# Kernel optimization log

Hardware: AMD Instinct MI355X
Metric: run time of the kernel (lower is better)

The kernel has to match this reference:

```python
import jax, jax.numpy as jnp
import numpy as np

D_MODEL = 1024
N_HEADS = 16
HEAD_DIM = D_MODEL // N_HEADS


def setup_inputs() -> dict:
    key = jax.random.key(0)
    ks = jax.random.split(key, 6)
    B, S = 2, 2048
    scale = 1.0 / np.sqrt(D_MODEL)
    x = jax.random.normal(ks[0], (B, S, D_MODEL), dtype=jnp.float32)
    Wq = jax.random.normal(ks[1], (D_MODEL, D_MODEL), dtype=jnp.float32) * scale
    Wk = jax.random.normal(ks[2], (D_MODEL, D_MODEL), dtype=jnp.float32) * scale
    Wv = jax.random.normal(ks[3], (D_MODEL, D_MODEL), dtype=jnp.float32) * scale
    Wo = jax.random.normal(ks[4], (D_MODEL, D_MODEL), dtype=jnp.float32) * scale
    bo = jax.random.normal(ks[5], (D_MODEL,), dtype=jnp.float32) * 0.02
    return {"x": x, "Wq": Wq, "Wk": Wk, "Wv": Wv, "Wo": Wo, "bo": bo}


def reference(x, Wq, Wk, Wv, Wo, bo):
    B, S, _ = x.shape
    H, hd = N_HEADS, HEAD_DIM
    # qkv projections (no bias, qkv_bias=False)
    q = (x @ Wq).reshape(B, S, H, hd).transpose(0, 2, 1, 3)  # [B,H,S,hd]
    k = (x @ Wk).reshape(B, S, H, hd).transpose(0, 2, 1, 3)
    v = (x @ Wv).reshape(B, S, H, hd).transpose(0, 2, 1, 3)
    scores = jnp.einsum('bhqd,bhkd->bhqk', q, k)  # [B,H,S,S]
    causal = jnp.tril(jnp.ones((S, S), dtype=bool))  # True = keep
    scores = jnp.where(causal, scores, -jnp.inf)
    weights = jax.nn.softmax(scores / np.sqrt(hd), axis=-1)
    # dropout p=0.0 -> identity
    ctx = jnp.einsum('bhqk,bhkd->bhqd', weights, v)  # [B,H,S,hd]
    ctx = ctx.transpose(0, 2, 1, 3).reshape(B, S, H * hd)
    return ctx @ Wo + bo
```

## Files before the change

### kernel.cpp

```cpp
#include <hip/hip_runtime.h>
#include <hip/hip_bf16.h>
#include <stdint.h>

#define SEQ    2048
#define BATCH  2
#define DMODEL 1024
#define NHEADS 16
#define HDIM   64
#define MROWS  (BATCH*SEQ)

typedef __attribute__((ext_vector_type(8))) short bf16x8;
typedef __attribute__((ext_vector_type(4))) short bf16x4;
typedef __attribute__((ext_vector_type(4))) float f32x4;

__device__ inline void global_to_lds16(const void* g, void* l) {
  __builtin_amdgcn_global_load_lds(
      (const __attribute__((address_space(1))) uint32_t*)g,
      (__attribute__((address_space(3))) uint32_t*)l, 16, 0, 0);
}

__device__ inline unsigned short f2bf_bits(float f) {
  __hip_bfloat16 h = __float2bfloat16(f);
  return *(unsigned short*)&h;
}

__global__ void prep_kernel(const float* __restrict__ x, __hip_bfloat16* __restrict__ xb,
                            const float* __restrict__ Wq, const float* __restrict__ Wk,
                            const float* __restrict__ Wv, const float* __restrict__ Wo,
                            __hip_bfloat16* __restrict__ Wqkv_t, __hip_bfloat16* __restrict__ Wo_t) {
  __shared__ float tile[32][33];
  if (blockIdx.x < 4096) {
    int i = (blockIdx.x * 256 + threadIdx.x) * 4;
    float4 v = *(const float4*)(x + i);
    ushort4 o;
    o.x = f2bf_bits(v.x); o.y = f2bf_bits(v.y);
    o.z = f2bf_bits(v.z); o.w = f2bf_bits(v.w);
    *(ushort4*)(xb + i) = o;
    return;
  }
  int idx = blockIdx.x - 4096;
  int z = idx >> 10;
  int rem = idx & 1023;
  const float* W = (z == 0) ? Wq : (z == 1) ? Wk : (z == 2) ? Wv : Wo;
  __hip_bfloat16* dst = (z < 3) ? (Wqkv_t + (size_t)z * 1024 * 1024) : Wo_t;
  int k0 = (rem & 31) * 32, n0 = (rem >> 5) * 32;
  int tx = threadIdx.x & 31, ty = threadIdx.x >> 5;
#pragma unroll
  for (int r = 0; r < 4; r++)
    tile[ty + r * 8][tx] = W[(size_t)(k0 + ty + r * 8) * 1024 + n0 + tx];
  __syncthreads();
#pragma unroll
  for (int r = 0; r < 4; r++)
    dst[(size_t)(n0 + ty + r * 8) * 1024 + k0 + tx] = __float2bfloat16(tile[tx][ty + r * 8]);
}

template <int TN, bool OUT_BF16, int MINW, bool FUSE_VT>
__global__ __launch_bounds__(256, MINW)
void gemm_kernel(const __hip_bfloat16* __restrict__ A, const __hip_bfloat16* __restrict__ Bt,
                 void* __restrict__ C, const float* __restrict__ bias, int ldc,
                 __hip_bfloat16* __restrict__ Vt) {
  __shared__ __hip_bfloat16 Asl[2][128 * 64];
  __shared__ __hip_bfloat16 Bsl[2][TN * 64];

  const int t = threadIdx.x;
  const int lane = t & 63;
  const int w = t >> 6;
  constexpr int MI = (TN == 128) ? 4 : 2;
  const int wrow = (TN == 128) ? (w >> 1) * 64 : w * 32;
  const int wcol = (TN == 128) ? (w & 1) * 64 : 0;
  const int m0 = blockIdx.y * 128;
  const int n0 = blockIdx.x * TN;

  f32x4 acc[MI][4];
#pragma unroll
  for (int i = 0; i < MI; i++)
#pragma unroll
    for (int j = 0; j < 4; j++) acc[i][j] = (f32x4){0.f, 0.f, 0.f, 0.f};

  const int srow = lane >> 3;
  const int sjc = (lane & 7) ^ srow;
  const int fm = lane & 15;
  const int g4 = lane >> 4;

  auto stage = [&](int k0, int bufi) {
#pragma unroll
    for (int i = 0; i < 4; i++) {
      int seg = i * 4 + w;
      int r = seg * 8 + srow;
      global_to_lds16(A + (size_t)(m0 + r) * 1024 + k0 + sjc * 8,
                      (void*)(&Asl[bufi][0] + seg * 512 + lane * 8));
    }
#pragma unroll
    for (int i = 0; i < TN / 32; i++) {
      int seg = i * 4 + w;
      int r = seg * 8 + srow;
      global_to_lds16(Bt + (size_t)(n0 + r) * 1024 + k0 + sjc * 8,
                      (void*)(&Bsl[bufi][0] + seg * 512 + lane * 8));
    }
  };

  stage(0, 0);
  for (int k0 = 0; k0 < 1024; k0 += 64) {
    const int buf = (k0 >> 6) & 1;
    __syncthreads();

    bf16x8 af[2][MI], bfr[2][4];
#pragma unroll
    for (int kb = 0; kb < 2; kb++) {
#pragma unroll
      for (int mi = 0; mi < MI; mi++) {
        int row = wrow + mi * 16 + fm;
        af[kb][mi] = *(const bf16x8*)(&Asl[buf][0] + row * 64 + (((kb * 4 + g4) ^ (row & 7)) << 3));
      }
#pragma unroll
      for (int ni = 0; ni < 4; ni++) {
        int row = wcol + ni * 16 + fm;
        bfr[kb][ni] = *(const bf16x8*)(&Bsl[buf][0] + row * 64 + (((kb * 4 + g4) ^ (row & 7)) << 3));
      }
    }

    if (k0 + 64 < 1024) stage(k0 + 64, buf ^ 1);

#pragma unroll
    for (int kb = 0; kb < 2; kb++)
#pragma unroll
      for (int mi = 0; mi < MI; mi++)
#pragma unroll
        for (int ni = 0; ni < 4; ni++)
          acc[mi][ni] = __builtin_amdgcn_mfma_f32_16x16x32_bf16(af[kb][mi], bfr[kb][ni], acc[mi][ni], 0, 0, 0);
  }

  const bool vt_block = FUSE_VT && (n0 >= 2048);
#pragma unroll
  for (int mi = 0; mi < MI; mi++) {
    int mb = m0 + wrow + mi * 16 + g4 * 4;
#pragma unroll
    for (int ni = 0; ni < 4; ni++) {
      int n = n0 + wcol + ni * 16 + fm;
      if (vt_block) {
        int nv = n - 2048;
        int bhh = (mb >> 11) * 16 + (nv >> 6);
        int d = nv & 63;
        int s = mb & 2047;
        unsigned short u[4];
#pragma unroll
        for (int r = 0; r < 4; r++) u[r] = f2bf_bits(acc[mi][ni][r]);
        *(ushort4*)(Vt + ((size_t)bhh * 64 + d) * 2048 + s) = *(const ushort4*)u;
      } else {
        float bv = OUT_BF16 ? 0.f : bias[n];
#pragma unroll
        for (int r = 0; r < 4; r++) {
          if (OUT_BF16)
            ((__hip_bfloat16*)C)[(size_t)(mb + r) * ldc + n] = __float2bfloat16(acc[mi][ni][r]);
          else
            ((float*)C)[(size_t)(mb + r) * ldc + n] = acc[mi][ni][r] + bv;
        }
      }
    }
  }
}

__global__ __launch_bounds__(256, 2)
void attn_kernel(const __hip_bfloat16* __restrict__ QKV,
                 const __hip_bfloat16* __restrict__ Vt,
                 __hip_bfloat16* __restrict__ ctx) {
  __shared__ __hip_bfloat16 Klds[2][128 * 64];
  __shared__ __hip_bfloat16 Vlds[2][64 * 128];

  const int t = threadIdx.x;
  const int lane = t & 63;
  const int w = t >> 6;
  const int L = blockIdx.x;
  const int bh = (L & 7) + 8 * ((L >> 3) & 3);
  const int jraw = L >> 5;
  const int jb = (jraw < 8) ? jraw : 23 - jraw;
  const int qtab[2] = { jb, 31 - jb };
  const int b = bh >> 4, h = bh & 15;
  const int fm = lane & 15;
  const int g4 = lane >> 4;
  const int fk = g4 * 8;
  const size_t rowb = (size_t)b * SEQ;
  const float c = 0.18033688011112042f;

  const int krr = lane >> 3;
  const int kjc = (lane & 7) ^ krr;
  const int vrr = lane >> 4;

  bf16x8 qf[2][2];
#pragma unroll
  for (int hh = 0; hh < 2; hh++) {
    const __hip_bfloat16* qp = QKV + (rowb + qtab[hh] * 64 + w * 16 + fm) * 3072 + h * 64 + fk;
    bf16x8 r0 = *(const bf16x8*)qp;
    bf16x8 r1 = *(const bf16x8*)(qp + 32);
#pragma unroll
    for (int i = 0; i < 8; i++) {
      float f0 = __uint_as_float(((unsigned)(unsigned short)r0[i]) << 16) * c;
      float f1 = __uint_as_float(((unsigned)(unsigned short)r1[i]) << 16) * c;
      r0[i] = (short)f2bf_bits(f0);
      r1[i] = (short)f2bf_bits(f1);
    }
    qf[hh][0] = r0; qf[hh][1] = r1;
  }

  bf16x4 ones4;
#pragma unroll
  for (int i = 0; i < 4; i++) ones4[i] = (short)0x3F80;

  f32x4 acc[2][4];
  f32x4 lacc[2];
#pragma unroll
  for (int hh = 0; hh < 2; hh++) {
    lacc[hh] = (f32x4){0.f, 0.f, 0.f, 0.f};
#pragma unroll
    for (int d = 0; d < 4; d++) acc[hh][d] = (f32x4){0.f, 0.f, 0.f, 0.f};
  }

  auto stage = [&](int pt, int bufi) {
    const int kt0 = pt * 128;
#pragma unroll
    for (int i = 0; i < 4; i++) {
      int seg = i * 4 + w;
      int kr = seg * 8 + krr;
      global_to_lds16(QKV + (rowb + kt0 + kr) * 3072 + 1024 + h * 64 + kjc * 8,
                      (void*)(&Klds[bufi][0] + seg * 512 + lane * 8));
      int vd = seg * 4 + vrr;
      int vjc = (lane & 15) ^ ((seg & 1) * 4 + vrr);
      global_to_lds16(Vt + ((size_t)bh * 64 + vd) * 2048 + kt0 + vjc * 8,
                      (void*)(&Vlds[bufi][0] + seg * 512 + lane * 8));
    }
  };

  auto subcompute = [&](const bf16x8 (&kf)[2][4], const bf16x4 (&vf)[4][4], int kts) {
    const bool act0 = (kts <= qtab[0]);
    f32x4 st1[4], st0[4];
#pragma unroll
    for (int ns = 0; ns < 4; ns++) {
      st1[ns] = (f32x4){0.f, 0.f, 0.f, 0.f};
      st0[ns] = (f32x4){0.f, 0.f, 0.f, 0.f};
    }
#pragma unroll
    for (int kk = 0; kk < 2; kk++) {
#pragma unroll
      for (int ns = 0; ns < 4; ns++)
        st1[ns] = __builtin_amdgcn_mfma_f32_16x16x32_bf16(kf[kk][ns], qf[1][kk], st1[ns], 0, 0, 0);
      if (act0)
#pragma unroll
        for (int ns = 0; ns < 4; ns++)
          st0[ns] = __builtin_amdgcn_mfma_f32_16x16x32_bf16(kf[kk][ns], qf[0][kk], st0[ns], 0, 0, 0);
    }
    auto half = [&](const f32x4 (&st)[4], int hh) {
      const bool diag = (kts == qtab[hh]);
#pragma unroll
      for (int ns = 0; ns < 4; ns++) {
        float e[4];
#pragma unroll
        for (int r = 0; r < 4; r++) {
          float p = __builtin_amdgcn_exp2f(st[ns][r]);
          if (diag) {
            int ktl = ns * 16 + g4 * 4 + r;
            p = (ktl > w * 16 + fm) ? 0.f : p;
          }
          e[r] = p;
        }
        unsigned lo = __builtin_amdgcn_perm(__builtin_bit_cast(unsigned, e[1]),
                                            __builtin_bit_cast(unsigned, e[0]), 0x07060302u);
        unsigned hi = __builtin_amdgcn_perm(__builtin_bit_cast(unsigned, e[3]),
                                            __builtin_bit_cast(unsigned, e[2]), 0x07060302u);
        uint2 pp; pp.x = lo; pp.y = hi;
        bf16x4 pf = __builtin_bit_cast(bf16x4, pp);
        lacc[hh] = __builtin_amdgcn_mfma_f32_16x16x16bf16_1k(pf, ones4, lacc[hh], 0, 0, 0);
#pragma unroll
        for (int dd = 0; dd < 4; dd++)
          acc[hh][dd] = __builtin_amdgcn_mfma_f32_16x16x16bf16_1k(pf, vf[dd][ns], acc[hh][dd], 0, 0, 0);
      }
    };
    half(st1, 1);
    if (act0) half(st0, 0);
  };

  auto load_kf = [&](const __hip_bfloat16* Kb, int sc, bf16x8 (&kf)[2][4]) {
#pragma unroll
    for (int kk = 0; kk < 2; kk++)
#pragma unroll
      for (int ns = 0; ns < 4; ns++) {
        int row = sc * 64 + ns * 16 + fm;
        kf[kk][ns] = *(const bf16x8*)(Kb + row * 64 + (((kk * 4 + g4) ^ (fm & 7)) << 3));
      }
  };
  auto load_vf = [&](const __hip_bfloat16* Vb, int sc, bf16x4 (&vf)[4][4]) {
#pragma unroll
    for (int dd = 0; dd < 4; dd++)
#pragma unroll
      for (int ns = 0; ns < 4; ns++) {
        int ch = sc * 8 + ns * 2 + (g4 >> 1);
        vf[dd][ns] = *(const bf16x4*)(Vb + (dd * 16 + fm) * 128 +
                                      ((ch ^ (fm & 7)) << 3) + (g4 & 1) * 4);
      }
  };

  const int lastt = qtab[1];
  const int lastp = lastt >> 1;
  stage(0, 0);
  for (int pt = 0; pt <= lastp; ++pt) {
    __syncthreads();
    const int buf = pt & 1;
    const __hip_bfloat16* Kb = &Klds[buf][0];
    const __hip_bfloat16* Vb = &Vlds[buf][0];

    bf16x8 kf[2][4];
    bf16x4 vf[4][4];
    load_kf(Kb, 0, kf);
    load_vf(Kb == Kb ? Vb : Vb, 0, vf);
    if (pt < lastp) stage(pt + 1, buf ^ 1);
    subcompute(kf, vf, pt * 2);

    if (pt * 2 + 1 <= lastt) {
      load_kf(Kb, 1, kf);
      load_vf(Vb, 1, vf);
      subcompute(kf, vf, pt * 2 + 1);
    }
  }

#pragma unroll
  for (int hh = 0; hh < 2; hh++) {
    float rl[4];
#pragma unroll
    for (int r = 0; r < 4; r++) rl[r] = __builtin_amdgcn_rcpf(lacc[hh][r]);
#pragma unroll
    for (int dd = 0; dd < 4; dd++)
#pragma unroll
      for (int r = 0; r < 4; r++) {
        int q = qtab[hh] * 64 + w * 16 + g4 * 4 + r;
        ctx[(rowb + q) * 1024 + h * 64 + dd * 16 + fm] =
            __float2bfloat16(acc[hh][dd][r] * rl[r]);
      }
  }
}

extern "C" void kernel_launch(void* const* d_in, const int* in_sizes, int n_in,
                              void* d_out, int out_size, void* d_ws, size_t ws_size,
                              hipStream_t stream) {
  const float* x  = (const float*)d_in[0];
  const float* Wq = (const float*)d_in[1];
  const float* Wk = (const float*)d_in[2];
  const float* Wv = (const float*)d_in[3];
  const float* Wo = (const float*)d_in[4];
  const float* bo = (const float*)d_in[5];
  float* out = (float*)d_out;

  char* ws = (char*)d_ws;
  __hip_bfloat16* xb     = (__hip_bfloat16*)(ws);
  __hip_bfloat16* Wqkv_t = (__hip_bfloat16*)(ws + (8ull  << 20));
  __hip_bfloat16* Wo_t   = (__hip_bfloat16*)(ws + (14ull << 20));
  __hip_bfloat16* QKV    = (__hip_bfloat16*)(ws + (16ull << 20));
  __hip_bfloat16* ctxb   = (__hip_bfloat16*)(ws + (40ull << 20));
  __hip_bfloat16* Vt     = (__hip_bfloat16*)(ws + (48ull << 20));

  prep_kernel<<<dim3(8192), dim3(256), 0, stream>>>(x, xb, Wq, Wk, Wv, Wo, Wqkv_t, Wo_t);
  gemm_kernel<128, true, 2, true><<<dim3(24, 32), dim3(256), 0, stream>>>(
      xb, Wqkv_t, (void*)QKV, nullptr, 3072, Vt);
  attn_kernel<<<dim3(512), dim3(256), 0, stream>>>(QKV, Vt, ctxb);
  gemm_kernel<64, false, 2, false><<<dim3(16, 32), dim3(256), 0, stream>>>(
      ctxb, Wo_t, (void*)out, bo, 1024, nullptr);
}
```

Baseline: 167.8 us.

## Add dedicated 256x256-tile QKV GEMM with 4-stage LDS pipeline

Replaces the generic 128-tile GEMM for the QKV projection with a specialized kernel using 512 threads, 256x256 output tiles, and a 4-stage global-to-LDS ring buffer. It splits each k-step into two MFMA half-phases, interleaving async loads with explicit waitcnt, barriers and setprio. The goal is to raise arithmetic intensity and hide memory latency. It needs 128KB of dynamic LDS, which limits occupancy, and grid 12x16=192 blocks may underfill the 256 CUs of the device.

New measurement: 170.1 us. About the same (+1.4%).

```diff
diff --git a/kernel.cpp b/kernel.cpp
--- a/kernel.cpp
+++ b/kernel.cpp
@@ -155,6 +155,137 @@
           else
             ((float*)C)[(size_t)(mb + r) * ldc + n] = acc[mi][ni][r] + bv;
         }
+      }
+    }
+  }
+}
+
+__global__ __launch_bounds__(512, 2)
+void qkv_gemm_kernel(const __hip_bfloat16* __restrict__ A,
+                     const __hip_bfloat16* __restrict__ Bt,
+                     __hip_bfloat16* __restrict__ QKV,
+                     __hip_bfloat16* __restrict__ Vt) {
+  extern __shared__ __align__(128) char smem_raw[];
+  __hip_bfloat16* Asl = (__hip_bfloat16*)smem_raw;
+  __hip_bfloat16* Bsl = Asl + 4 * 8192;
+
+  const int t = threadIdx.x;
+  const int lane = t & 63;
+  const int w = t >> 6;
+  const int wm = w >> 2;
+  const int wn = w & 3;
+
+  const int wgid = blockIdx.y * 12 + blockIdx.x;
+  const int swz = (wgid & 7) * 24 + (wgid >> 3);
+  const int m0 = (swz / 12) * 256;
+  const int n0 = (swz % 12) * 256;
+
+  const int fm = lane & 15;
+  const int g4 = lane >> 4;
+  const int rsl = ((g4 ^ ((fm >> 1) & 3)) << 3);
+  const int rr = lane >> 2;
+  const int cc = (lane & 3) ^ ((lane >> 3) & 3);
+
+  f32x4 acc[8][4];
+#pragma unroll
+  for (int i = 0; i < 8; i++)
+#pragma unroll
+    for (int j = 0; j < 4; j++) acc[i][j] = (f32x4){0.f, 0.f, 0.f, 0.f};
+
+  auto stageA = [&](int ktt, int s) {
+#pragma unroll
+    for (int i = 0; i < 2; i++) {
+      int seg = w * 2 + i;
+      global_to_lds16(A + (size_t)(m0 + seg * 16 + rr) * 1024 + ktt * 32 + cc * 8,
+                      (void*)(Asl + s * 8192 + seg * 512 + lane * 8));
+    }
+  };
+  auto stageB = [&](int ktt, int s) {
+#pragma unroll
+    for (int i = 0; i < 2; i++) {
+      int seg = w * 2 + i;
+      global_to_lds16(Bt + (size_t)(n0 + seg * 16 + rr) * 1024 + ktt * 32 + cc * 8,
+                      (void*)(Bsl + s * 8192 + seg * 512 + lane * 8));
+    }
+  };
+
+  stageA(0, 0); stageB(0, 0);
+  stageA(1, 1); stageB(1, 1);
+  stageA(2, 2); stageB(2, 2);
+  asm volatile("s_waitcnt vmcnt(8)" ::: "memory");
+  __builtin_amdgcn_s_barrier();
+
+  for (int kt = 0; kt < 32; ++kt) {
+    const int s = kt & 3;
+    const __hip_bfloat16* Ab = Asl + s * 8192;
+    const __hip_bfloat16* Bb = Bsl + s * 8192;
+
+    bf16x8 af[4], bf[4];
+#pragma unroll
+    for (int mi = 0; mi < 4; mi++) {
+      int row = wm * 128 + mi * 16 + fm;
+      af[mi] = *(const bf16x8*)(Ab + row * 32 + rsl);
+    }
+#pragma unroll
+    for (int ni = 0; ni < 4; ni++) {
+      int row = wn * 64 + ni * 16 + fm;
+      bf[ni] = *(const bf16x8*)(Bb + row * 32 + rsl);
+    }
+    if (kt < 29) stageA(kt + 3, (kt + 3) & 3);
+    __builtin_amdgcn_s_barrier();
+    __builtin_amdgcn_sched_barrier(0);
+    __builtin_amdgcn_s_setprio(1);
+#pragma unroll
+    for (int mi = 0; mi < 4; mi++)
+#pragma unroll
+      for (int ni = 0; ni < 4; ni++)
+        acc[mi][ni] = __builtin_amdgcn_mfma_f32_16x16x32_bf16(af[mi], bf[ni], acc[mi][ni], 0, 0, 0);
+    __builtin_amdgcn_s_setprio(0);
+    __builtin_amdgcn_sched_barrier(0);
+    __builtin_amdgcn_s_barrier();
+
+#pragma unroll
+    for (int mi = 0; mi < 4; mi++) {
+      int row = wm * 128 + (mi + 4) * 16 + fm;
+      af[mi] = *(const bf16x8*)(Ab + row * 32 + rsl);
+    }
+    if (kt < 29) stageB(kt + 3, (kt + 3) & 3);
+    __builtin_amdgcn_s_barrier();
+    __builtin_amdgcn_sched_barrier(0);
+    __builtin_amdgcn_s_setprio(1);
+#pragma unroll
+    for (int mi = 0; mi < 4; mi++)
+#pragma unroll
+      for (int ni = 0; ni < 4; ni++)
+        acc[mi + 4][ni] = __builtin_amdgcn_mfma_f32_16x16x32_bf16(af[mi], bf[ni], acc[mi + 4][ni], 0, 0, 0);
+    __builtin_amdgcn_s_setprio(0);
+    __builtin_amdgcn_sched_barrier(0);
+    if (kt < 29)       asm volatile("s_waitcnt vmcnt(8)" ::: "memory");
+    else if (kt == 29) asm volatile("s_waitcnt vmcnt(4)" ::: "memory");
+    else if (kt == 30) asm volatile("s_waitcnt vmcnt(0)" ::: "memory");
+    __builtin_amdgcn_s_barrier();
+  }
+
+  const bool vt_block = (n0 >= 2048);
+#pragma unroll
+  for (int mi = 0; mi < 8; mi++) {
+    int mb = m0 + wm * 128 + mi * 16 + g4 * 4;
+#pragma unroll
+    for (int ni = 0; ni < 4; ni++) {
+      int n = n0 + wn * 64 + ni * 16 + fm;
+      if (vt_block) {
+        int nv = n - 2048;
+        int bhh = (mb >> 11) * 16 + (nv >> 6);
+        int d = nv & 63;
+        int ssq = mb & 2047;
+        unsigned short u[4];
+#pragma unroll
+        for (int r = 0; r < 4; r++) u[r] = f2bf_bits(acc[mi][ni][r]);
+        *(ushort4*)(Vt + ((size_t)bhh * 64 + d) * 2048 + ssq) = *(const ushort4*)u;
+      } else {
+#pragma unroll
+        for (int r = 0; r < 4; r++)
+          QKV[(size_t)(mb + r) * 3072 + n] = __float2bfloat16(acc[mi][ni][r]);
       }
     }
   }
@@ -310,7 +441,7 @@
     bf16x8 kf[2][4];
     bf16x4 vf[4][4];
     load_kf(Kb, 0, kf);
-    load_vf(Kb == Kb ? Vb : Vb, 0, vf);
+    load_vf(Vb, 0, vf);
     if (pt < lastp) stage(pt + 1, buf ^ 1);
     subcompute(kf, vf, pt * 2);
 
@@ -356,9 +487,15 @@
   __hip_bfloat16* ctxb   = (__hip_bfloat16*)(ws + (40ull << 20));
   __hip_bfloat16* Vt     = (__hip_bfloat16*)(ws + (48ull << 20));
 
+  static int qkv_attr_done = 0;
+  if (!qkv_attr_done) {
+    (void)hipFuncSetAttribute((const void*)qkv_gemm_kernel,
+                              hipFuncAttributeMaxDynamicSharedMemorySize, 131072);
+    qkv_attr_done = 1;
+  }
+
   prep_kernel<<<dim3(8192), dim3(256), 0, stream>>>(x, xb, Wq, Wk, Wv, Wo, Wqkv_t, Wo_t);
-  gemm_kernel<128, true, 2, true><<<dim3(24, 32), dim3(256), 0, stream>>>(
-      xb, Wqkv_t, (void*)QKV, nullptr, 3072, Vt);
+  qkv_gemm_kernel<<<dim3(12, 16), dim3(512), 131072, stream>>>(xb, Wqkv_t, QKV, Vt);
   attn_kernel<<<dim3(512), dim3(256), 0, stream>>>(QKV, Vt, ctxb);
   gemm_kernel<64, false, 2, false><<<dim3(16, 32), dim3(256), 0, stream>>>(
       ctxb, Wo_t, (void*)out, bo, 1024, nullptr);
```
